# Optimization experiments

Hardware: AMD Instinct MI355X
Metric: run time of the kernel (lower is better)

Reference implementation:

```python
import jax, jax.numpy as jnp
import numpy as np

USER = 100000
ITEM = 50000
N = USER + ITEM
LATDIM = 64
IMG_DIM = 1024
E_ADJ = 3_000_000
E_IMG = 1_000_000
GNN_LAYERS = 2
RIS_LAMBDA = 1.0
EPS = 1e-12


def spmm(rows, cols, vals, x):
    # sparse [N,N] @ dense [N,D] via gather + segment-sum
    return jax.ops.segment_sum(vals[:, None] * x[cols], rows, num_segments=N)


def setup_inputs() -> dict:
    key = jax.random.key(0)
    ks = jax.random.split(key, 10)
    return {
        "adj_rows": jax.random.randint(ks[0], (E_ADJ,), 0, N, dtype=jnp.int32),
        "adj_cols": jax.random.randint(ks[1], (E_ADJ,), 0, N, dtype=jnp.int32),
        "adj_vals": jax.random.uniform(ks[2], (E_ADJ,), dtype=jnp.float32),
        "img_rows": jax.random.randint(ks[3], (E_IMG,), 0, N, dtype=jnp.int32),
        "img_cols": jax.random.randint(ks[4], (E_IMG,), 0, N, dtype=jnp.int32),
        "img_vals": jax.random.uniform(ks[5], (E_IMG,), dtype=jnp.float32),
        "image_embedding": jax.random.normal(ks[6], (ITEM, IMG_DIM), dtype=jnp.float32),
        "uEmbeds": jax.random.normal(ks[7], (USER, LATDIM), dtype=jnp.float32) * 0.01,
        "iEmbeds": jax.random.normal(ks[8], (ITEM, LATDIM), dtype=jnp.float32) * 0.01,
        "W_trans": jax.random.normal(ks[9], (IMG_DIM, LATDIM), dtype=jnp.float32) * (1.0 / np.sqrt(IMG_DIM)),
        "b_trans": jnp.zeros((LATDIM,), dtype=jnp.float32),
    }


def reference(adj_rows, adj_cols, adj_vals, img_rows, img_cols, img_vals,
              image_embedding, uEmbeds, iEmbeds, W_trans, b_trans):
    # trans == 1: Linear projection of image features
    image_feats = image_embedding @ W_trans + b_trans  # [ITEM, LATDIM]

    # image_adj @ concat(u, i)
    embeds_img_adj = spmm(img_rows, img_cols, img_vals, jnp.concatenate([uEmbeds, iEmbeds], axis=0))

    # F.normalize(image_feats) along dim=1 (L2, eps=1e-12)
    nrm = jnp.linalg.norm(image_feats, axis=1, keepdims=True)
    feats_n = image_feats / jnp.maximum(nrm, EPS)

    embeds_image = spmm(adj_rows, adj_cols, adj_vals, jnp.concatenate([uEmbeds, feats_n], axis=0))
    embeds_image_ = spmm(adj_rows, adj_cols, adj_vals,
                         jnp.concatenate([embeds_image[:USER], iEmbeds], axis=0))
    embeds_image = embeds_image + embeds_image_ + RIS_LAMBDA * embeds_img_adj

    # stacked GCN layers with sum over all layer outputs (including input)
    acc = embeds_image
    cur = embeds_image
    for _ in range(GNN_LAYERS):
        cur = spmm(adj_rows, adj_cols, adj_vals, cur)
        acc = acc + cur

    return acc[:USER], acc[USER:]
```

## Files before the change

kernel.cpp:

```cpp
#include <hip/hip_runtime.h>
#include <hip/hip_fp16.h>

#define USER_N 100000
#define ITEM_N 50000
#define NN (USER_N + ITEM_N)
#define D 64
#define IMGD 1024
#define LDP 68

#define BUCKET_BITS 10
#define BROWS (1 << BUCKET_BITS)
#define NBUCK ((NN + BROWS - 1) >> BUCKET_BITS)
#define CHUNK 4096

typedef _Float16 v4h __attribute__((ext_vector_type(4)));
typedef _Float16 v8h __attribute__((ext_vector_type(8)));
typedef float v4f __attribute__((ext_vector_type(4)));

__global__ __launch_bounds__(256) void wt_prep(
    const float* __restrict__ W, _Float16* __restrict__ Wt16)
{
    const int id = blockIdx.x * 256 + threadIdx.x;
    if (id >= D * IMGD) return;
    const int c = id >> 10;
    const int k = id & 1023;
    Wt16[id] = (_Float16)W[(size_t)k * D + c];
}

__global__ __launch_bounds__(256) void gemm_mfma3(
    const float* __restrict__ A, const _Float16* __restrict__ Wt16,
    const float* __restrict__ b, float* __restrict__ C)
{
    const int t = threadIdx.x;
    const int gwave = (blockIdx.x * 256 + t) >> 6;
    const int lane = t & 63;
    const int l16 = lane & 15;
    const int g = lane >> 4;
    const int row0 = gwave * 16;
    if (row0 >= ITEM_N) return;
    const int arow = row0 + l16;
    const bool rv = arow < ITEM_N;
    const float* ap = A + (size_t)arow * IMGD + g * 4;
    const _Float16* wbase = Wt16 + (size_t)l16 * IMGD + g * 4;

    v4f acc[4] = {};

    float4 a[4];
#pragma unroll
    for (int j = 0; j < 4; j++) a[j] = make_float4(0.f, 0.f, 0.f, 0.f);
    if (rv) {
#pragma unroll
        for (int j = 0; j < 4; j++)
            a[j] = *reinterpret_cast<const float4*>(ap + j * 16);
    }

    for (int k0 = 0; k0 < IMGD; k0 += 64) {
        float4 na[4];
#pragma unroll
        for (int j = 0; j < 4; j++) na[j] = make_float4(0.f, 0.f, 0.f, 0.f);
        if (rv && (k0 + 64) < IMGD) {
#pragma unroll
            for (int j = 0; j < 4; j++)
                na[j] = *reinterpret_cast<const float4*>(ap + k0 + 64 + j * 16);
        }
        union { v8h v; v4h h[2]; } af0, af1;
        {
            v4h h;
            h[0] = (_Float16)a[0].x; h[1] = (_Float16)a[0].y;
            h[2] = (_Float16)a[0].z; h[3] = (_Float16)a[0].w;
            af0.h[0] = h;
            h[0] = (_Float16)a[1].x; h[1] = (_Float16)a[1].y;
            h[2] = (_Float16)a[1].z; h[3] = (_Float16)a[1].w;
            af0.h[1] = h;
            h[0] = (_Float16)a[2].x; h[1] = (_Float16)a[2].y;
            h[2] = (_Float16)a[2].z; h[3] = (_Float16)a[2].w;
            af1.h[0] = h;
            h[0] = (_Float16)a[3].x; h[1] = (_Float16)a[3].y;
            h[2] = (_Float16)a[3].z; h[3] = (_Float16)a[3].w;
            af1.h[1] = h;
        }
#pragma unroll
        for (int n = 0; n < 4; n++) {
            const _Float16* wp = wbase + (size_t)(n * 16) * IMGD + k0;
            union { v8h v; v4h h[2]; } bf;
            bf.h[0] = *reinterpret_cast<const v4h*>(wp);
            bf.h[1] = *reinterpret_cast<const v4h*>(wp + 16);
            acc[n] = __builtin_amdgcn_mfma_f32_16x16x32_f16(af0.v, bf.v, acc[n], 0, 0, 0);
        }
#pragma unroll
        for (int n = 0; n < 4; n++) {
            const _Float16* wp = wbase + (size_t)(n * 16) * IMGD + k0 + 32;
            union { v8h v; v4h h[2]; } bf;
            bf.h[0] = *reinterpret_cast<const v4h*>(wp);
            bf.h[1] = *reinterpret_cast<const v4h*>(wp + 16);
            acc[n] = __builtin_amdgcn_mfma_f32_16x16x32_f16(af1.v, bf.v, acc[n], 0, 0, 0);
        }
#pragma unroll
        for (int j = 0; j < 4; j++) a[j] = na[j];
    }
#pragma unroll
    for (int n = 0; n < 4; n++) {
        const int col = n * 16 + l16;
        const float bias = b[col];
#pragma unroll
        for (int r = 0; r < 4; r++) {
            const int grow = row0 + g * 4 + r;
            if (grow < ITEM_N)
                C[(size_t)grow * D + col] = acc[n][r] + bias;
        }
    }
}

__global__ __launch_bounds__(256) void gemm_feats32(
    const float* __restrict__ A, const float* __restrict__ W,
    const float* __restrict__ b, float* __restrict__ C)
{
    __shared__ float As[32][LDP];
    __shared__ float Ws[64][LDP];
    const int row0 = blockIdx.x * 32;
    const int t = threadIdx.x;
    const int tx = t & 15, ty = t >> 4;
    float acc[2][4] = {};

    const int lr = t >> 4;
    const int lk = (t & 15) * 4;

    for (int k0 = 0; k0 < IMGD; k0 += 64) {
#pragma unroll
        for (int i = 0; i < 2; i++) {
            const int r = lr + i * 16;
            const int grow = row0 + r;
            float4 v = make_float4(0.f, 0.f, 0.f, 0.f);
            if (grow < ITEM_N)
                v = *reinterpret_cast<const float4*>(&A[(size_t)grow * IMGD + k0 + lk]);
            *reinterpret_cast<float4*>(&As[r][lk]) = v;
        }
#pragma unroll
        for (int i = 0; i < 4; i++) {
            const int kr = lr + i * 16;
            float4 v = *reinterpret_cast<const float4*>(&W[(size_t)(k0 + kr) * D + lk]);
            *reinterpret_cast<float4*>(&Ws[kr][lk]) = v;
        }
        __syncthreads();
#pragma unroll
        for (int kb = 0; kb < 16; kb++) {
            float a_[2][4], w_[4][4];
#pragma unroll
            for (int i = 0; i < 2; i++) {
                const float4 v = *reinterpret_cast<const float4*>(&As[ty * 2 + i][kb * 4]);
                a_[i][0] = v.x; a_[i][1] = v.y; a_[i][2] = v.z; a_[i][3] = v.w;
            }
#pragma unroll
            for (int j = 0; j < 4; j++) {
                const float4 v = *reinterpret_cast<const float4*>(&Ws[kb * 4 + j][tx * 4]);
                w_[j][0] = v.x; w_[j][1] = v.y; w_[j][2] = v.z; w_[j][3] = v.w;
            }
#pragma unroll
            for (int j = 0; j < 4; j++)
#pragma unroll
                for (int i = 0; i < 2; i++)
#pragma unroll
                    for (int c = 0; c < 4; c++)
                        acc[i][c] += a_[i][j] * w_[j][c];
        }
        __syncthreads();
    }
    const float4 bias = *reinterpret_cast<const float4*>(&b[tx * 4]);
#pragma unroll
    for (int i = 0; i < 2; i++) {
        const int grow = row0 + ty * 2 + i;
        if (grow < ITEM_N) {
            float4 v;
            v.x = acc[i][0] + bias.x;
            v.y = acc[i][1] + bias.y;
            v.z = acc[i][2] + bias.z;
            v.w = acc[i][3] + bias.w;
            *reinterpret_cast<float4*>(&C[(size_t)grow * D + tx * 4]) = v;
        }
    }
}

__global__ __launch_bounds__(256) void rownorm_h(
    const float* __restrict__ X, __half* __restrict__ Y, int nrows)
{
    const int gid = blockIdx.x * blockDim.x + threadIdx.x;
    const int row = gid >> 6;
    const int lane = threadIdx.x & 63;
    if (row >= nrows) return;
    float v = X[(size_t)row * D + lane];
    float s = v * v;
#pragma unroll
    for (int o = 32; o > 0; o >>= 1) s += __shfl_xor(s, o, 64);
    const float scale = 1.0f / fmaxf(sqrtf(s), 1e-12f);
    Y[(size_t)row * D + lane] = __float2half(v * scale);
}

__global__ __launch_bounds__(256) void rownorm(float* __restrict__ X, int nrows)
{
    const int gid = blockIdx.x * blockDim.x + threadIdx.x;
    const int row = gid >> 6;
    const int lane = threadIdx.x & 63;
    if (row >= nrows) return;
    float v = X[(size_t)row * D + lane];
    float s = v * v;
#pragma unroll
    for (int o = 32; o > 0; o >>= 1) s += __shfl_xor(s, o, 64);
    const float scale = 1.0f / fmaxf(sqrtf(s), 1e-12f);
    X[(size_t)row * D + lane] = v * scale;
}

__global__ __launch_bounds__(256) void cvt_f2h(
    const float* __restrict__ s, __half* __restrict__ d, int n4)
{
    const int i = blockIdx.x * blockDim.x + threadIdx.x;
    if (i >= n4) return;
    const float4 v = reinterpret_cast<const float4*>(s)[i];
    __half2* d2 = reinterpret_cast<__half2*>(d);
    d2[2 * i]     = __floats2half2_rn(v.x, v.y);
    d2[2 * i + 1] = __floats2half2_rn(v.z, v.w);
}

__global__ __launch_bounds__(256) void bucket_count(
    const int* __restrict__ rows, int nnz, int nb, int* __restrict__ histT)
{
    __shared__ int cnt[NBUCK];
    for (int i = threadIdx.x; i < NBUCK; i += 256) cnt[i] = 0;
    __syncthreads();
    const int e0 = blockIdx.x * CHUNK;
    const int e1 = min(e0 + CHUNK, nnz);
    for (int e = e0 + threadIdx.x; e < e1; e += 256)
        atomicAdd(&cnt[rows[e] >> BUCKET_BITS], 1);
    __syncthreads();
    for (int b = threadIdx.x; b < NBUCK; b += 256)
        histT[b * nb + blockIdx.x] = cnt[b];
}

__global__ __launch_bounds__(1024) void scanA(
    const int* __restrict__ cnt, int* __restrict__ excl,
    int* __restrict__ blocksums, int n)
{
    const int t = threadIdx.x;
    const int gid = blockIdx.x * 1024 + t;
    const int lane = t & 63, wid = t >> 6;
    int v = (gid < n) ? cnt[gid] : 0;
    int x = v;
#pragma unroll
    for (int o = 1; o < 64; o <<= 1) {
        int y = __shfl_up(x, o, 64);
        if (lane >= o) x += y;
    }
    __shared__ int ws[16];
    __shared__ int wo[16];
    if (lane == 63) ws[wid] = x;
    __syncthreads();
    if (t < 16) {
        int s = ws[t];
        int xx = s;
#pragma unroll
        for (int o = 1; o < 16; o <<= 1) {
            int y = __shfl_up(xx, o, 16);
            if (t >= o) xx += y;
        }
        wo[t] = xx - s;
        if (t == 15) blocksums[blockIdx.x] = xx;
    }
    __syncthreads();
    if (gid < n) excl[gid] = x - v + wo[wid];
}

__global__ __launch_bounds__(1024) void scanB(int* __restrict__ bs, int nb)
{
    const int t = threadIdx.x;
    const int lane = t & 63, wid = t >> 6;
    int v = (t < nb) ? bs[t] : 0;
    int x = v;
#pragma unroll
    for (int o = 1; o < 64; o <<= 1) {
        int y = __shfl_up(x, o, 64);
        if (lane >= o) x += y;
    }
    __shared__ int ws[16];
    __shared__ int wo[16];
    if (lane == 63) ws[wid] = x;
    __syncthreads();
    if (t < 16) {
        int s = ws[t];
        int xx = s;
#pragma unroll
        for (int o = 1; o < 16; o <<= 1) {
            int y = __shfl_up(xx, o, 16);
            if (t >= o) xx += y;
        }
        wo[t] = xx - s;
    }
    __syncthreads();
    if (t < nb) bs[t] = x - v + wo[wid];
}

__global__ __launch_bounds__(256) void scan_apply(
    int* __restrict__ excl, const int* __restrict__ bo, int n)
{
    const int gid = blockIdx.x * blockDim.x + threadIdx.x;
    if (gid < n) excl[gid] += bo[gid >> 10];
}

__global__ __launch_bounds__(256) void bucket_place(
    const int* __restrict__ rows, const int* __restrict__ cols,
    const float* __restrict__ vals, int nnz, int nb,
    const int* __restrict__ offsT, uint2* __restrict__ rec)
{
    __shared__ int cur[NBUCK];
    for (int b = threadIdx.x; b < NBUCK; b += 256)
        cur[b] = offsT[b * nb + blockIdx.x];
    __syncthreads();
    const int e0 = blockIdx.x * CHUNK;
    const int e1 = min(e0 + CHUNK, nnz);
    for (int e = e0 + threadIdx.x; e < e1; e += 256) {
        const int r = rows[e];
        const int b = r >> BUCKET_BITS;
        const int pos = atomicAdd(&cur[b], 1);
        rec[pos] = make_uint2(((unsigned)cols[e] << BUCKET_BITS) |
                                  (unsigned)(r & (BROWS - 1)),
                              __float_as_uint(vals[e]));
    }
}

__global__ __launch_bounds__(1024) void bucket_finalize(
    const uint2* __restrict__ rec, int nnz, int nb,
    const int* __restrict__ offsT, int* __restrict__ rp,
    int2* __restrict__ ev)
{
    const int b = blockIdx.x;
    const int t = threadIdx.x;
    const int rlo = b << BUCKET_BITS;
    const int segs = offsT[b * nb];
    const int sege = (b + 1 < NBUCK) ? offsT[(b + 1) * nb] : nnz;

    __shared__ int cnt[BROWS];
    __shared__ int cur[BROWS];
    cnt[t] = 0;
    __syncthreads();
    for (int i = segs + t; i < sege; i += 1024)
        atomicAdd(&cnt[rec[i].x & (BROWS - 1)], 1);
    __syncthreads();

    const int lane = t & 63, wid = t >> 6;
    const int v = cnt[t];
    int x = v;
#pragma unroll
    for (int o = 1; o < 64; o <<= 1) {
        int y = __shfl_up(x, o, 64);
        if (lane >= o) x += y;
    }
    __shared__ int wsum[16];
    __shared__ int woff[16];
    if (lane == 63) wsum[wid] = x;
    __syncthreads();
    if (t < 16) {
        int s = wsum[t];
        int xx = s;
#pragma unroll
        for (int o = 1; o < 16; o <<= 1) {
            int y = __shfl_up(xx, o, 16);
            if (t >= o) xx += y;
        }
        woff[t] = xx - s;
    }
    __syncthreads();
    const int start = segs + (x - v + woff[wid]);

    if (rlo + t < NN) rp[rlo + t] = start;
    if (b == NBUCK - 1 && t == 0) rp[NN] = nnz;
    cur[t] = start;
    __syncthreads();

    for (int i = segs + t; i < sege; i += 1024) {
        const uint2 R = rec[i];
        const int rl = (int)(R.x & (BROWS - 1));
        const int c = (int)(R.x >> BUCKET_BITS);
        const int pos = atomicAdd(&cur[rl], 1);
        ev[pos] = make_int2(c, (int)R.y);
    }
}

__global__ __launch_bounds__(256) void spmm_h8(
    const int* __restrict__ rp, const int2* __restrict__ ev,
    const __half* __restrict__ src,
    float* __restrict__ out32, __half* __restrict__ out16, int limit16,
    const float* __restrict__ add1, const float* __restrict__ add2)
{
    const int wid = (blockIdx.x * 256 + threadIdx.x) >> 6;
    const int lane = threadIdx.x & 63;
    const int sub = lane >> 3;
    const int l8 = lane & 7;
    const int rowbase = wid * 8;
    if (rowbase >= NN) return;
    const int row = rowbase + sub;

    int v = 0;
    if (lane <= 8 && rowbase + lane <= NN) v = rp[rowbase + lane];
    const int s = __shfl(v, sub, 64);
    const int e = __shfl(v, sub + 1, 64);

    const __half* srcl = src + l8 * 8;
    float acc[8] = {};

    union cvt4 { uint4 u; __half2 h[4]; };
    int i = s;
    for (; i + 3 < e; i += 4) {
        const int2 E0 = ev[i], E1 = ev[i + 1], E2 = ev[i + 2], E3 = ev[i + 3];
        cvt4 g0, g1, g2, g3;
        g0.u = *reinterpret_cast<const uint4*>(srcl + (size_t)E0.x * D);
        g1.u = *reinterpret_cast<const uint4*>(srcl + (size_t)E1.x * D);
        g2.u = *reinterpret_cast<const uint4*>(srcl + (size_t)E2.x * D);
        g3.u = *reinterpret_cast<const uint4*>(srcl + (size_t)E3.x * D);
#pragma unroll
        for (int k = 0; k < 4; k++) {
            const cvt4& g = k == 0 ? g0 : k == 1 ? g1 : k == 2 ? g2 : g3;
            const float w = __int_as_float(k == 0 ? E0.y : k == 1 ? E1.y
                                           : k == 2 ? E2.y : E3.y);
#pragma unroll
            for (int j = 0; j < 4; j++) {
                const float2 f = __half22float2(g.h[j]);
                acc[2 * j]     += w * f.x;
                acc[2 * j + 1] += w * f.y;
            }
        }
    }
    for (; i < e; i++) {
        const int2 E0 = ev[i];
        cvt4 g;
        g.u = *reinterpret_cast<const uint4*>(srcl + (size_t)E0.x * D);
        const float w = __int_as_float(E0.y);
#pragma unroll
        for (int j = 0; j < 4; j++) {
            const float2 f = __half22float2(g.h[j]);
            acc[2 * j]     += w * f.x;
            acc[2 * j + 1] += w * f.y;
        }
    }

    if (row >= NN) return;
    const size_t idx = (size_t)row * D + l8 * 8;
#pragma unroll
    for (int h = 0; h < 2; h++) {
        if (add1) {
            const float4 a = *reinterpret_cast<const float4*>(&add1[idx + h * 4]);
            acc[4 * h] += a.x; acc[4 * h + 1] += a.y;
            acc[4 * h + 2] += a.z; acc[4 * h + 3] += a.w;
        }
        if (add2) {
            const float4 a = *reinterpret_cast<const float4*>(&add2[idx + h * 4]);
            acc[4 * h] += a.x; acc[4 * h + 1] += a.y;
            acc[4 * h + 2] += a.z; acc[4 * h + 3] += a.w;
        }
        float4 o;
        o.x = acc[4 * h]; o.y = acc[4 * h + 1];
        o.z = acc[4 * h + 2]; o.w = acc[4 * h + 3];
        *reinterpret_cast<float4*>(&out32[idx + h * 4]) = o;
    }
    if (row < limit16) {
        cvt4 o16;
#pragma unroll
        for (int j = 0; j < 4; j++)
            o16.h[j] = __floats2half2_rn(acc[2 * j], acc[2 * j + 1]);
        *reinterpret_cast<uint4*>(&out16[idx]) = o16.u;
    }
}

__global__ __launch_bounds__(256) void spmm_csr(
    const int* __restrict__ rp, const int2* __restrict__ ev,
    const float* __restrict__ srcU, const float* __restrict__ srcI,
    float* __restrict__ out,
    const float* __restrict__ add1, const float* __restrict__ add2)
{
    const int gid = blockIdx.x * blockDim.x + threadIdx.x;
    const int row = gid >> 6;
    const int lane = threadIdx.x & 63;
    if (row >= NN) return;
    const int s = rp[row], e = rp[row + 1];
    float acc = 0.f;
    int i = s;
    for (; i + 3 < e; i += 4) {
        const int2 e0 = ev[i], e1 = ev[i + 1], e2 = ev[i + 2], e3 = ev[i + 3];
        const float* p0 = (e0.x < USER_N) ? (srcU + (size_t)e0.x * D)
                                          : (srcI + (size_t)(e0.x - USER_N) * D);
        const float* p1 = (e1.x < USER_N) ? (srcU + (size_t)e1.x * D)
                                          : (srcI + (size_t)(e1.x - USER_N) * D);
        const float* p2 = (e2.x < USER_N) ? (srcU + (size_t)e2.x * D)
                                          : (srcI + (size_t)(e2.x - USER_N) * D);
        const float* p3 = (e3.x < USER_N) ? (srcU + (size_t)e3.x * D)
                                          : (srcI + (size_t)(e3.x - USER_N) * D);
        acc += __int_as_float(e0.y) * p0[lane];
        acc += __int_as_float(e1.y) * p1[lane];
        acc += __int_as_float(e2.y) * p2[lane];
        acc += __int_as_float(e3.y) * p3[lane];
    }
    for (; i < e; i++) {
        const int2 e0 = ev[i];
        const float* p0 = (e0.x < USER_N) ? (srcU + (size_t)e0.x * D)
                                          : (srcI + (size_t)(e0.x - USER_N) * D);
        acc += __int_as_float(e0.y) * p0[lane];
    }
    const size_t idx = (size_t)row * D + lane;
    if (add1) acc += add1[idx];
    if (add2) acc += add2[idx];
    out[idx] = acc;
}

extern "C" void kernel_launch(void* const* d_in, const int* in_sizes, int n_in,
                              void* d_out, int out_size, void* d_ws, size_t ws_size,
                              hipStream_t stream)
{
    const int*   adj_rows = (const int*)d_in[0];
    const int*   adj_cols = (const int*)d_in[1];
    const float* adj_vals = (const float*)d_in[2];
    const int*   img_rows = (const int*)d_in[3];
    const int*   img_cols = (const int*)d_in[4];
    const float* img_vals = (const float*)d_in[5];
    const float* img_emb  = (const float*)d_in[6];
    const float* uEmb     = (const float*)d_in[7];
    const float* iEmb     = (const float*)d_in[8];
    const float* Wt       = (const float*)d_in[9];
    const float* bt       = (const float*)d_in[10];
    float* out = (float*)d_out;

    const int e_adj = in_sizes[0];
    const int e_img = in_sizes[3];
    const int e_max = e_adj > e_img ? e_adj : e_img;
    const int NB_adj = (e_adj + CHUNK - 1) / CHUNK;
    const int NB_img = (e_img + CHUNK - 1) / CHUNK;
    const int NB_max = NB_adj > NB_img ? NB_adj : NB_img;

    const size_t ndbytes = (size_t)NN * D * sizeof(float);
    const size_t nhbytes = (size_t)NN * D * sizeof(__half);

    size_t off = 0;
    auto carve = [&](size_t bytes) { size_t p = off; off += (bytes + 255) & ~(size_t)255; return p; };
    char* base = (char*)d_ws;
    const size_t o_featsN = carve((size_t)ITEM_N * D * sizeof(float));
    const size_t o_bufA   = carve(ndbytes);
    const size_t o_bufB   = carve(ndbytes);
    const size_t o_rpAdj  = carve((NN + 1) * sizeof(int));
    const size_t o_rpImg  = carve((NN + 1) * sizeof(int));
    const size_t o_bsums  = carve(1024 * sizeof(int));
    const size_t o_histT  = carve((size_t)NBUCK * NB_max * sizeof(int));
    const size_t o_rec    = carve((size_t)e_max * sizeof(uint2) > nhbytes
                                      ? (size_t)e_max * sizeof(uint2) : nhbytes);
    const size_t o_evAdj  = carve((size_t)e_adj * sizeof(int2));
    const size_t need_base = off;
    const size_t o_evImg  = carve((size_t)e_img * sizeof(int2) > nhbytes
                                      ? (size_t)e_img * sizeof(int2) : nhbytes);
    const size_t o_x0     = carve(nhbytes);
    const size_t o_wt16   = carve((size_t)D * IMGD * sizeof(_Float16));
    const size_t need_h = off;

    if (ws_size < need_base) return;
    const bool use_h = (ws_size >= need_h);

    float* featsN = (float*)(base + o_featsN);
    float* bufA   = (float*)(base + o_bufA);
    float* bufB   = (float*)(base + o_bufB);
    int* rpAdj    = (int*)(base + o_rpAdj);
    int* rpImg    = (int*)(base + o_rpImg);
    int* bsums    = (int*)(base + o_bsums);
    int* histT    = (int*)(base + o_histT);
    uint2* rec    = (uint2*)(base + o_rec);
    int2* evAdj   = (int2*)(base + o_evAdj);
    int2* evImg   = (int2*)(base + o_evImg);
    __half* xC    = (__half*)(base + o_rec);
    __half* xB    = (__half*)(base + o_evImg);
    __half* x0    = (__half*)(base + o_x0);
    _Float16* wt16 = (_Float16*)(base + o_wt16);

    {
        const int n = NBUCK * NB_adj;
        const int nsb = (n + 1023) / 1024;
        bucket_count<<<NB_adj, 256, 0, stream>>>(adj_rows, e_adj, NB_adj, histT);
        scanA<<<nsb, 1024, 0, stream>>>(histT, histT, bsums, n);
        scanB<<<1, 1024, 0, stream>>>(bsums, nsb);
        scan_apply<<<(n + 255) / 256, 256, 0, stream>>>(histT, bsums, n);
        bucket_place<<<NB_adj, 256, 0, stream>>>(
            adj_rows, adj_cols, adj_vals, e_adj, NB_adj, histT, rec);
        bucket_finalize<<<NBUCK, 1024, 0, stream>>>(
            rec, e_adj, NB_adj, histT, rpAdj, evAdj);
    }
    {
        const int n = NBUCK * NB_img;
        const int nsb = (n + 1023) / 1024;
        bucket_count<<<NB_img, 256, 0, stream>>>(img_rows, e_img, NB_img, histT);
        scanA<<<nsb, 1024, 0, stream>>>(histT, histT, bsums, n);
        scanB<<<1, 1024, 0, stream>>>(bsums, nsb);
        scan_apply<<<(n + 255) / 256, 256, 0, stream>>>(histT, bsums, n);
        bucket_place<<<NB_img, 256, 0, stream>>>(
            img_rows, img_cols, img_vals, e_img, NB_img, histT, rec);
        bucket_finalize<<<NBUCK, 1024, 0, stream>>>(
            rec, e_img, NB_img, histT, rpImg, evImg);
    }

    const int SPMM8_GRID = (NN + 31) / 32;
    const int SPMM_GRID = (NN * 64 + 255) / 256;
    const int RN_GRID = (ITEM_N * 64 + 255) / 256;
    const int GEMM3_GRID = ((ITEM_N + 15) / 16 + 3) / 4;

    if (use_h) {
        __half* x0I = x0 + (size_t)USER_N * D;
        __half* xBI = xB + (size_t)USER_N * D;

        cvt_f2h<<<(USER_N * D / 4 + 255) / 256, 256, 0, stream>>>(
            uEmb, x0, USER_N * D / 4);
        cvt_f2h<<<(ITEM_N * D / 4 + 255) / 256, 256, 0, stream>>>(
            iEmb, x0I, ITEM_N * D / 4);

        spmm_h8<<<SPMM8_GRID, 256, 0, stream>>>(
            rpImg, evImg, x0, bufA, nullptr, 0, nullptr, nullptr);

        wt_prep<<<(D * IMGD + 255) / 256, 256, 0, stream>>>(Wt, wt16);
        gemm_mfma3<<<GEMM3_GRID, 256, 0, stream>>>(img_emb, wt16, bt, featsN);
        rownorm_h<<<RN_GRID, 256, 0, stream>>>(featsN, x0I, ITEM_N);

        cvt_f2h<<<(ITEM_N * D / 4 + 255) / 256, 256, 0, stream>>>(
            iEmb, xBI, ITEM_N * D / 4);

        spmm_h8<<<SPMM8_GRID, 256, 0, stream>>>(
            rpAdj, evAdj, x0, bufB, xB, USER_N, nullptr, nullptr);

        spmm_h8<<<SPMM8_GRID, 256, 0, stream>>>(
            rpAdj, evAdj, xB, bufA, xC, NN, bufB, bufA);

        spmm_h8<<<SPMM8_GRID, 256, 0, stream>>>(
            rpAdj, evAdj, xC, bufB, x0, NN, nullptr, nullptr);

        spmm_h8<<<SPMM8_GRID, 256, 0, stream>>>(
            rpAdj, evAdj, x0, out, nullptr, 0, bufA, bufB);
    } else {
        gemm_feats32<<<(ITEM_N + 31) / 32, 256, 0, stream>>>(img_emb, Wt, bt, featsN);
        rownorm<<<RN_GRID, 256, 0, stream>>>(featsN, ITEM_N);

        spmm_csr<<<SPMM_GRID, 256, 0, stream>>>(
            rpImg, evImg, uEmb, iEmb, bufA, nullptr, nullptr);
        spmm_csr<<<SPMM_GRID, 256, 0, stream>>>(
            rpAdj, evAdj, uEmb, featsN, bufB, nullptr, nullptr);
        spmm_csr<<<SPMM_GRID, 256, 0, stream>>>(
            rpAdj, evAdj, bufB, iEmb, bufA, bufB, bufA);
        spmm_csr<<<SPMM_GRID, 256, 0, stream>>>(
            rpAdj, evAdj, bufA, bufA + (size_t)USER_N * D, bufB, nullptr, nullptr);
        spmm_csr<<<SPMM_GRID, 256, 0, stream>>>(
            rpAdj, evAdj, bufB, bufB + (size_t)USER_N * D, out, bufA, bufB);
    }
}
```

Baseline: 622.7 us.

## Split-K the image projection GEMM and merge fp16 conversion launches

The MFMA projection GEMM now splits the 1024-long K dimension four ways. Each wave computes a 16-row strip over a quarter of K and writes a partial result. A new rownorm kernel sums the four partials, adds the bias and normalizes, giving four times as many waves to hide the latency of streaming the 200MB image matrix. The three separate fp32→fp16 conversion launches are merged into a single kernel that also writes the item copy into xB. The cost is extra partial-buffer traffic (reusing bufB), and the GEMM drops its register prefetch and the bounds checks, which depend on ITEM_N being divisible by 16.

Result: faster. 599.2 us (-3.8%).

```diff
diff --git a/kernel.cpp b/kernel.cpp
--- a/kernel.cpp
+++ b/kernel.cpp
@@ -7,6 +7,7 @@
 #define D 64
 #define IMGD 1024
 #define LDP 68
+#define KSPLIT 4
 
 #define BUCKET_BITS 10
 #define BROWS (1 << BUCKET_BITS)
@@ -27,42 +28,33 @@
     Wt16[id] = (_Float16)W[(size_t)k * D + c];
 }
 
-__global__ __launch_bounds__(256) void gemm_mfma3(
+__global__ __launch_bounds__(256) void gemm_mfma5(
     const float* __restrict__ A, const _Float16* __restrict__ Wt16,
-    const float* __restrict__ b, float* __restrict__ C)
+    float* __restrict__ P0, float* __restrict__ P123)
 {
     const int t = threadIdx.x;
     const int gwave = (blockIdx.x * 256 + t) >> 6;
+    const int nstrip = ITEM_N / 16;
+    if (gwave >= nstrip * KSPLIT) return;
+    const int strip = gwave >> 2;
+    const int ks = gwave & (KSPLIT - 1);
+    const int row0 = strip * 16;
     const int lane = t & 63;
     const int l16 = lane & 15;
     const int g = lane >> 4;
-    const int row0 = gwave * 16;
-    if (row0 >= ITEM_N) return;
-    const int arow = row0 + l16;
-    const bool rv = arow < ITEM_N;
-    const float* ap = A + (size_t)arow * IMGD + g * 4;
+    const int kbase = ks * (IMGD / KSPLIT);
+
+    const float* ap = A + (size_t)(row0 + l16) * IMGD + g * 4;
     const _Float16* wbase = Wt16 + (size_t)l16 * IMGD + g * 4;
 
     v4f acc[4] = {};
 
-    float4 a[4];
-#pragma unroll
-    for (int j = 0; j < 4; j++) a[j] = make_float4(0.f, 0.f, 0.f, 0.f);
-    if (rv) {
+    for (int c = 0; c < IMGD / KSPLIT; c += 64) {
+        const int k0 = kbase + c;
+        float4 a[4];
 #pragma unroll
         for (int j = 0; j < 4; j++)
-            a[j] = *reinterpret_cast<const float4*>(ap + j * 16);
-    }
-
-    for (int k0 = 0; k0 < IMGD; k0 += 64) {
-        float4 na[4];
-#pragma unroll
-        for (int j = 0; j < 4; j++) na[j] = make_float4(0.f, 0.f, 0.f, 0.f);
-        if (rv && (k0 + 64) < IMGD) {
-#pragma unroll
-            for (int j = 0; j < 4; j++)
-                na[j] = *reinterpret_cast<const float4*>(ap + k0 + 64 + j * 16);
-        }
+            a[j] = *reinterpret_cast<const float4*>(ap + k0 + j * 16);
         union { v8h v; v4h h[2]; } af0, af1;
         {
             v4h h;
@@ -86,27 +78,19 @@
             bf.h[0] = *reinterpret_cast<const v4h*>(wp);
             bf.h[1] = *reinterpret_cast<const v4h*>(wp + 16);
             acc[n] = __builtin_amdgcn_mfma_f32_16x16x32_f16(af0.v, bf.v, acc[n], 0, 0, 0);
-        }
-#pragma unroll
-        for (int n = 0; n < 4; n++) {
-            const _Float16* wp = wbase + (size_t)(n * 16) * IMGD + k0 + 32;
-            union { v8h v; v4h h[2]; } bf;
-            bf.h[0] = *reinterpret_cast<const v4h*>(wp);
-            bf.h[1] = *reinterpret_cast<const v4h*>(wp + 16);
+            bf.h[0] = *reinterpret_cast<const v4h*>(wp + 32);
+            bf.h[1] = *reinterpret_cast<const v4h*>(wp + 48);
             acc[n] = __builtin_amdgcn_mfma_f32_16x16x32_f16(af1.v, bf.v, acc[n], 0, 0, 0);
         }
-#pragma unroll
-        for (int j = 0; j < 4; j++) a[j] = na[j];
-    }
+    }
+    float* Cp = (ks == 0) ? P0 : P123 + (size_t)(ks - 1) * ITEM_N * D;
 #pragma unroll
     for (int n = 0; n < 4; n++) {
         const int col = n * 16 + l16;
-        const float bias = b[col];
 #pragma unroll
         for (int r = 0; r < 4; r++) {
             const int grow = row0 + g * 4 + r;
-            if (grow < ITEM_N)
-                C[(size_t)grow * D + col] = acc[n][r] + bias;
+            Cp[(size_t)grow * D + col] = acc[n][r];
         }
     }
 }
@@ -180,8 +164,25 @@
     }
 }
 
-__global__ __launch_bounds__(256) void rownorm_h(
-    const float* __restrict__ X, __half* __restrict__ Y, int nrows)
+__global__ __launch_bounds__(256) void rownorm_h4(
+    const float* __restrict__ P0, const float* __restrict__ P123,
+    const float* __restrict__ b, __half* __restrict__ Y, int nrows)
+{
+    const int gid = blockIdx.x * blockDim.x + threadIdx.x;
+    const int row = gid >> 6;
+    const int lane = threadIdx.x & 63;
+    if (row >= nrows) return;
+    const size_t idx = (size_t)row * D + lane;
+    const size_t N1 = (size_t)ITEM_N * D;
+    float v = P0[idx] + P123[idx] + P123[idx + N1] + P123[idx + 2 * N1] + b[lane];
+    float s = v * v;
+#pragma unroll
+    for (int o = 32; o > 0; o >>= 1) s += __shfl_xor(s, o, 64);
+    const float scale = 1.0f / fmaxf(sqrtf(s), 1e-12f);
+    Y[idx] = __float2half(v * scale);
+}
+
+__global__ __launch_bounds__(256) void rownorm(float* __restrict__ X, int nrows)
 {
     const int gid = blockIdx.x * blockDim.x + threadIdx.x;
     const int row = gid >> 6;
@@ -192,32 +193,25 @@
 #pragma unroll
     for (int o = 32; o > 0; o >>= 1) s += __shfl_xor(s, o, 64);
     const float scale = 1.0f / fmaxf(sqrtf(s), 1e-12f);
-    Y[(size_t)row * D + lane] = __float2half(v * scale);
-}
-
-__global__ __launch_bounds__(256) void rownorm(float* __restrict__ X, int nrows)
-{
-    const int gid = blockIdx.x * blockDim.x + threadIdx.x;
-    const int row = gid >> 6;
-    const int lane = threadIdx.x & 63;
-    if (row >= nrows) return;
-    float v = X[(size_t)row * D + lane];
-    float s = v * v;
-#pragma unroll
-    for (int o = 32; o > 0; o >>= 1) s += __shfl_xor(s, o, 64);
-    const float scale = 1.0f / fmaxf(sqrtf(s), 1e-12f);
     X[(size_t)row * D + lane] = v * scale;
 }
 
-__global__ __launch_bounds__(256) void cvt_f2h(
-    const float* __restrict__ s, __half* __restrict__ d, int n4)
-{
-    const int i = blockIdx.x * blockDim.x + threadIdx.x;
+__global__ __launch_bounds__(256) void cvt_x0(
+    const float* __restrict__ uE, const float* __restrict__ iE,
+    __half* __restrict__ x0, __half* __restrict__ xBI)
+{
+    const int i = blockIdx.x * 256 + threadIdx.x;
+    const int n4u = USER_N * D / 4;
+    const int n4 = NN * D / 4;
     if (i >= n4) return;
-    const float4 v = reinterpret_cast<const float4*>(s)[i];
-    __half2* d2 = reinterpret_cast<__half2*>(d);
-    d2[2 * i]     = __floats2half2_rn(v.x, v.y);
-    d2[2 * i + 1] = __floats2half2_rn(v.z, v.w);
+    const float4 v = (i < n4u) ? reinterpret_cast<const float4*>(uE)[i]
+                               : reinterpret_cast<const float4*>(iE)[i - n4u];
+    union { uint2 u2; __half2 h[2]; } o;
+    o.h[0] = __floats2half2_rn(v.x, v.y);
+    o.h[1] = __floats2half2_rn(v.z, v.w);
+    *reinterpret_cast<uint2*>(x0 + (size_t)i * 4) = o.u2;
+    if (i >= n4u)
+        *reinterpret_cast<uint2*>(xBI + (size_t)(i - n4u) * 4) = o.u2;
 }
 
 __global__ __launch_bounds__(256) void bucket_count(
@@ -601,26 +595,20 @@
     const int SPMM8_GRID = (NN + 31) / 32;
     const int SPMM_GRID = (NN * 64 + 255) / 256;
     const int RN_GRID = (ITEM_N * 64 + 255) / 256;
-    const int GEMM3_GRID = ((ITEM_N + 15) / 16 + 3) / 4;
+    const int GEMM5_GRID = (ITEM_N / 16) * KSPLIT / 4;
 
     if (use_h) {
         __half* x0I = x0 + (size_t)USER_N * D;
         __half* xBI = xB + (size_t)USER_N * D;
 
-        cvt_f2h<<<(USER_N * D / 4 + 255) / 256, 256, 0, stream>>>(
-            uEmb, x0, USER_N * D / 4);
-        cvt_f2h<<<(ITEM_N * D / 4 + 255) / 256, 256, 0, stream>>>(
-            iEmb, x0I, ITEM_N * D / 4);
+        cvt_x0<<<(NN * D / 4 + 255) / 256, 256, 0, stream>>>(uEmb, iEmb, x0, xBI);
 
         spmm_h8<<<SPMM8_GRID, 256, 0, stream>>>(
             rpImg, evImg, x0, bufA, nullptr, 0, nullptr, nullptr);
 
         wt_prep<<<(D * IMGD + 255) / 256, 256, 0, stream>>>(Wt, wt16);
-        gemm_mfma3<<<GEMM3_GRID, 256, 0, stream>>>(img_emb, wt16, bt, featsN);
-        rownorm_h<<<RN_GRID, 256, 0, stream>>>(featsN, x0I, ITEM_N);
-
-        cvt_f2h<<<(ITEM_N * D / 4 + 255) / 256, 256, 0, stream>>>(
-            iEmb, xBI, ITEM_N * D / 4);
+        gemm_mfma5<<<GEMM5_GRID, 256, 0, stream>>>(img_emb, wt16, featsN, bufB);
+        rownorm_h4<<<RN_GRID, 256, 0, stream>>>(featsN, bufB, bt, x0I, ITEM_N);
 
         spmm_h8<<<SPMM8_GRID, 256, 0, stream>>>(
             rpAdj, evAdj, x0, bufB, xB, USER_N, nullptr, nullptr);
```
